# Optimization experiments

Hardware: AMD Instinct MI355X
Metric: run time of the kernel (lower is better)

Reference implementation:

```python
import jax, jax.numpy as jnp
import numpy as np

FEATURES_DIM = 64 * (64 * 10 + 1)  # 41024
BASE = 64 * 10 + 1                 # 641
B = 1024


def encode_boards(boards):
    """Vectorized HalfKP encode. boards: [B,8,8] int in 0..12.
    0 = my king, 12 = opp king, 6 = empty, 1..5 my pieces, 7..11 opp pieces.
    Returns [B, 2*FEATURES_DIM] float32 = concat(opps, mys) per original code."""
    nb = boards.shape[0]
    d = boards.reshape(nb, 64)
    sq = jnp.arange(64, dtype=jnp.int32)
    my_king = jnp.argmax(d == 0, axis=1).astype(jnp.int32)    # [B]
    opp_king = jnp.argmax(d == 12, axis=1).astype(jnp.int32)  # [B]
    is_my = (d >= 1) & (d <= 5)
    is_opp = (d >= 7) & (d <= 11)
    # MY_PIECE_TYPES index = piece-1 ; OPP_PIECE_TYPES [11,10,9,8,7] index = 11-piece
    my_idx = my_king[:, None] * BASE + (d - 1) * 64 + sq
    opp_idx = opp_king[:, None] * BASE + (11 - d) * 64 + sq
    my_idx = jnp.where(is_my, my_idx, FEATURES_DIM)    # out-of-range -> dropped
    opp_idx = jnp.where(is_opp, opp_idx, FEATURES_DIM)
    rows = jnp.arange(nb)[:, None]
    mys = jnp.zeros((nb, FEATURES_DIM), jnp.float32).at[rows, my_idx].set(1.0, mode='drop')
    opps = jnp.zeros((nb, FEATURES_DIM), jnp.float32).at[rows, opp_idx].set(1.0, mode='drop')
    return jnp.concatenate([opps, mys], axis=1)


def setup_inputs() -> dict:
    key = jax.random.key(0)
    ks = jax.random.split(key, 12)
    # boards: values 1..11 everywhere, then place exactly one my-king (0) and one opp-king (12)
    bf = jax.random.randint(ks[0], (B, 64), 1, 12, dtype=jnp.int32)
    mk = jax.random.randint(ks[1], (B,), 0, 32)
    ok = jax.random.randint(ks[2], (B,), 32, 64)
    rows = jnp.arange(B)
    bf = bf.at[rows, mk].set(0).at[rows, ok].set(12)
    boards = bf.reshape(B, 8, 8)
    s = 0.02
    W_my = jax.random.normal(ks[3], (256, FEATURES_DIM), jnp.float32) * s
    b_my = jax.random.normal(ks[4], (256,), jnp.float32) * s
    W_opp = jax.random.normal(ks[5], (256, FEATURES_DIM), jnp.float32) * s
    b_opp = jax.random.normal(ks[6], (256,), jnp.float32) * s
    W1 = jax.random.normal(ks[7], (32, 512), jnp.float32) * s
    b1 = jnp.zeros((32,), jnp.float32)
    W2 = jax.random.normal(ks[8], (32, 32), jnp.float32) * s
    b2 = jnp.zeros((32,), jnp.float32)
    W3 = jax.random.normal(ks[9], (1, 32), jnp.float32) * s
    b3 = jnp.zeros((1,), jnp.float32)
    return {"boards": boards, "W_my": W_my, "b_my": b_my, "W_opp": W_opp,
            "b_opp": b_opp, "W1": W1, "b1": b1, "W2": W2, "b2": b2,
            "W3": W3, "b3": b3}


def reference(boards, W_my, b_my, W_opp, b_opp, W1, b1, W2, b2, W3, b3):
    feats = encode_boards(boards)              # [B, 2*FEATURES_DIM] = (opps, mys)
    # NOTE: faithful to original: my_pieces consumes the FIRST half (which is opps)
    my_in = feats[:, :FEATURES_DIM]
    opp_in = feats[:, FEATURES_DIM:]
    my_pos = jax.nn.relu(my_in @ W_my.T + b_my)     # [B,256]
    opp_pos = jax.nn.relu(opp_in @ W_opp.T + b_opp) # [B,256]
    h = jnp.concatenate([my_pos, opp_pos], axis=1)  # [B,512]
    h = jax.nn.relu(h @ W1.T + b1)
    h = jax.nn.relu(h @ W2.T + b2)
    out = h @ W3.T + b3                             # [B,1]
    return out.reshape(-1)
```

## Files before the change

### kernel.cpp

```cpp
#include <hip/hip_runtime.h>

#define FD     41024
#define KBASE  641
#define WIN    320
#define SLDS   324
#define NB_MAX 1024

#define WS_OFF0  0
#define WS_OFF1  (NB_MAX*64)
#define WS_N0    (2*NB_MAX*64)
#define WS_N1    (WS_N0 + NB_MAX)
#define WS_KMY   (WS_N1 + NB_MAX)
#define WS_KOPP  (WS_KMY + NB_MAX)
#define WS_H     (WS_KOPP + NB_MAX)

__global__ __launch_bounds__(64) void classify(
    const int* __restrict__ boards, int* __restrict__ ws)
{
    __shared__ int s_off0[64], s_off1[64];
    __shared__ int s_cnt[2], s_k[2];
    const int b = blockIdx.x;
    const int t = threadIdx.x;

    s_off0[t] = 0; s_off1[t] = 0;
    if (t < 2) s_cnt[t] = 0;
    __syncthreads();

    const int d = boards[b * 64 + t];
    if (d == 0)       s_k[0] = t;
    else if (d == 12) s_k[1] = t;
    else if (d >= 1 && d <= 5) { int p = atomicAdd(&s_cnt[1], 1); s_off1[p] = (d - 1) * 64 + t; }
    else if (d >= 7 && d <= 11){ int p = atomicAdd(&s_cnt[0], 1); s_off0[p] = (11 - d) * 64 + t; }
    __syncthreads();

    ws[WS_OFF0 + b * 64 + t] = s_off0[t];
    ws[WS_OFF1 + b * 64 + t] = s_off1[t];
    if (t == 0) {
        ws[WS_N0   + b] = s_cnt[0];
        ws[WS_N1   + b] = s_cnt[1];
        ws[WS_KMY  + b] = s_k[0];
        ws[WS_KOPP + b] = s_k[1];
    }
}

__global__ __launch_bounds__(256) void gather_bucketed(
    const float* __restrict__ W_my, const float* __restrict__ W_opp,
    const float* __restrict__ b_my, const float* __restrict__ b_opp,
    const int* __restrict__ ws, float* __restrict__ h, int nb)
{
    __shared__ float win[32 * SLDS];
    __shared__ int   s_list[NB_MAX];
    __shared__ int   goffs[8 * 64];
    __shared__ int   s_cnt;

    const int blk = blockIdx.x;
    const int rg  = blk & 7;
    const int k   = (blk >> 3) & 63;
    const int m   = blk >> 9;
    const int t   = threadIdx.x;

    if (t == 0) s_cnt = 0;
    __syncthreads();

    const int* __restrict__ karr = ws + (m ? WS_KMY : WS_KOPP);
    for (int i = t; i < nb; i += 256)
        if (karr[i] == k) { int p = atomicAdd(&s_cnt, 1); s_list[p] = i; }
    __syncthreads();

    const int n_b = s_cnt;
    if (n_b == 0) return;

    const int shift = (k * KBASE) & 3;
    const int cs    = k * KBASE - shift;
    const float* __restrict__ W = m ? W_opp : W_my;
    const size_t gbase = (size_t)(rg * 32) * FD + (size_t)cs;
    #pragma unroll
    for (int u = 0; u < 11; u++) {
        const int idx = u * 256 + t;
        if (idx < 2592) {
            const int r  = idx / 81;
            const int c4 = idx - r * 81;
            const float4 v = *(const float4*)(W + gbase + (size_t)r * FD + c4 * 4);
            *(float4*)(&win[r * SLDS + c4 * 4]) = v;
        }
    }
    __syncthreads();

    const int* __restrict__ offarr = ws + (m ? WS_OFF1 : WS_OFF0);
    const int* __restrict__ narr   = ws + (m ? WS_N1   : WS_N0);
    const int r    = t & 31;
    const int slot = t >> 5;
    const float bias = (m ? b_opp : b_my)[rg * 32 + r];
    const int hcol = m * 256 + rg * 32 + r;
    const float* __restrict__ wrow = &win[r * SLDS + shift];

    for (int g = 0; g < n_b; g += 8) {
        {
            const int j  = t;
            if (j < 128) {
                const int bi = g + (j >> 4);
                if (bi < n_b) {
                    const int4 v = *(const int4*)(offarr + s_list[bi] * 64 + (j & 15) * 4);
                    *(int4*)(&goffs[j * 4]) = v;
                }
            }
        }
        __syncthreads();

        const int bi = g + slot;
        if (bi < n_b) {
            const int board = s_list[bi];
            const int nf = narr[board];
            const int* __restrict__ lo = &goffs[slot * 64];
            float acc0 = 0.0f, acc1 = 0.0f;
            int i = 0;
            for (; i + 4 <= nf; i += 4) {
                acc0 += wrow[lo[i]]     + wrow[lo[i + 1]];
                acc1 += wrow[lo[i + 2]] + wrow[lo[i + 3]];
            }
            for (; i < nf; i++) acc0 += wrow[lo[i]];
            h[(size_t)board * 512 + hcol] = fmaxf(acc0 + acc1 + bias, 0.0f);
        }
        __syncthreads();
    }
}

__global__ __launch_bounds__(256) void mlp_tail(
    const float* __restrict__ h,
    const float* __restrict__ W1, const float* __restrict__ b1,
    const float* __restrict__ W2, const float* __restrict__ b2,
    const float* __restrict__ W3, const float* __restrict__ b3,
    float* __restrict__ out)
{
    __shared__ float s_h[512];
    __shared__ float s_h1[32];
    const int b = blockIdx.x;
    const int t = threadIdx.x;

    s_h[t]       = h[(size_t)b * 512 + t];
    s_h[256 + t] = h[(size_t)b * 512 + 256 + t];
    __syncthreads();

    {
        const int o = t >> 3, l = t & 7;
        const float* __restrict__ w = W1 + o * 512;
        float p = 0.0f;
        for (int kk = l; kk < 512; kk += 8) p += s_h[kk] * w[kk];
        p += __shfl_down(p, 4, 8);
        p += __shfl_down(p, 2, 8);
        p += __shfl_down(p, 1, 8);
        if (l == 0) s_h1[o] = fmaxf(p + b1[o], 0.0f);
    }
    __syncthreads();

    if (t < 32) {
        const float* __restrict__ w = W2 + t * 32;
        float acc = b2[t];
        for (int kk = 0; kk < 32; kk++) acc += s_h1[kk] * w[kk];
        float h2 = fmaxf(acc, 0.0f);
        float p = h2 * W3[t];
        p += __shfl_down(p, 16, 32);
        p += __shfl_down(p,  8, 32);
        p += __shfl_down(p,  4, 32);
        p += __shfl_down(p,  2, 32);
        p += __shfl_down(p,  1, 32);
        if (t == 0) out[b] = p + b3[0];
    }
}

__global__ __launch_bounds__(256) void nnue_fwd(
    const int*   __restrict__ boards,
    const float* __restrict__ W_my,  const float* __restrict__ b_my,
    const float* __restrict__ W_opp, const float* __restrict__ b_opp,
    const float* __restrict__ W1,    const float* __restrict__ b1,
    const float* __restrict__ W2,    const float* __restrict__ b2,
    const float* __restrict__ W3,    const float* __restrict__ b3,
    float* __restrict__ out)
{
    __shared__ int   s_off0[64], s_off1[64];
    __shared__ int   s_cnt[2], s_kings[2];
    __shared__ float s_h[512];
    __shared__ float s_h1[32];

    const int b = blockIdx.x;
    const int t = threadIdx.x;

    if (t < 2) s_cnt[t] = 0;
    __syncthreads();

    if (t < 64) {
        int d = boards[b * 64 + t];
        if (d == 0)       s_kings[0] = t;
        else if (d == 12) s_kings[1] = t;
        else if (d >= 1 && d <= 5) { int p = atomicAdd(&s_cnt[1], 1); s_off1[p] = (d - 1) * 64 + t; }
        else if (d >= 7)           { int p = atomicAdd(&s_cnt[0], 1); s_off0[p] = (11 - d) * 64 + t; }
    }
    __syncthreads();

    const int n0 = s_cnt[0], n1 = s_cnt[1];
    const int base0 = s_kings[1] * KBASE;
    const int base1 = s_kings[0] * KBASE;

    {
        const float* __restrict__ w = W_my + (size_t)t * FD + base0;
        float acc = b_my[t];
        for (int i = 0; i < n0; i++) acc += w[s_off0[i]];
        s_h[t] = fmaxf(acc, 0.0f);
    }
    {
        const float* __restrict__ w = W_opp + (size_t)t * FD + base1;
        float acc = b_opp[t];
        for (int i = 0; i < n1; i++) acc += w[s_off1[i]];
        s_h[256 + t] = fmaxf(acc, 0.0f);
    }
    __syncthreads();

    {
        const int o = t >> 3, l = t & 7;
        const float* __restrict__ w = W1 + o * 512;
        float p = 0.0f;
        for (int kk = l; kk < 512; kk += 8) p += s_h[kk] * w[kk];
        p += __shfl_down(p, 4, 8);
        p += __shfl_down(p, 2, 8);
        p += __shfl_down(p, 1, 8);
        if (l == 0) s_h1[o] = fmaxf(p + b1[o], 0.0f);
    }
    __syncthreads();

    if (t < 32) {
        const float* __restrict__ w = W2 + t * 32;
        float acc = b2[t];
        for (int kk = 0; kk < 32; kk++) acc += s_h1[kk] * w[kk];
        float h2 = fmaxf(acc, 0.0f);
        float p = h2 * W3[t];
        p += __shfl_down(p, 16, 32);
        p += __shfl_down(p,  8, 32);
        p += __shfl_down(p,  4, 32);
        p += __shfl_down(p,  2, 32);
        p += __shfl_down(p,  1, 32);
        if (t == 0) out[b] = p + b3[0];
    }
}

extern "C" void kernel_launch(void* const* d_in, const int* in_sizes, int n_in,
                              void* d_out, int out_size, void* d_ws, size_t ws_size,
                              hipStream_t stream) {
    const int*   boards = (const int*)  d_in[0];
    const float* W_my   = (const float*)d_in[1];
    const float* b_my   = (const float*)d_in[2];
    const float* W_opp  = (const float*)d_in[3];
    const float* b_opp  = (const float*)d_in[4];
    const float* W1     = (const float*)d_in[5];
    const float* b1     = (const float*)d_in[6];
    const float* W2     = (const float*)d_in[7];
    const float* b2     = (const float*)d_in[8];
    const float* W3     = (const float*)d_in[9];
    const float* b3     = (const float*)d_in[10];
    float* out = (float*)d_out;

    const int nb = in_sizes[0] / 64;
    const size_t ws_needed = (size_t)(WS_H + (size_t)NB_MAX * 512) * sizeof(int);

    if (nb <= NB_MAX && ws_size >= ws_needed) {
        int*   wsi = (int*)d_ws;
        float* h   = (float*)d_ws + WS_H;
        classify<<<nb, 64, 0, stream>>>(boards, wsi);
        gather_bucketed<<<1024, 256, 0, stream>>>(W_my, W_opp, b_my, b_opp, wsi, h, nb);
        mlp_tail<<<nb, 256, 0, stream>>>(h, W1, b1, W2, b2, W3, b3, out);
    } else {
        nnue_fwd<<<nb, 256, 0, stream>>>(boards, W_my, b_my, W_opp, b_opp,
                                         W1, b1, W2, b2, W3, b3, out);
    }
}
```

Measured before the change: 145.5 us.

## Halve row group per block and prefetch weight window before bucket scan

Each gather block now covers 16 weight rows instead of 32, so twice as many blocks launch (2048) and each stages a smaller LDS window and processes 16 boards per group. The weight-window global loads are issued into registers before the king-bucket scan, so their latency overlaps the list build rather than following it. The cost is more blocks each re-scanning the king array and loading board offsets, extra registers for the prefetched float4s, and loads issued even for blocks that then exit with an empty bucket.

```diff
diff --git a/kernel.cpp b/kernel.cpp
--- a/kernel.cpp
+++ b/kernel.cpp
@@ -4,6 +4,7 @@
 #define KBASE  641
 #define WIN    320
 #define SLDS   324
+#define ROWG   16
 #define NB_MAX 1024
 
 #define WS_OFF0  0
@@ -48,20 +49,35 @@
     const float* __restrict__ b_my, const float* __restrict__ b_opp,
     const int* __restrict__ ws, float* __restrict__ h, int nb)
 {
-    __shared__ float win[32 * SLDS];
+    __shared__ float win[ROWG * SLDS];
     __shared__ int   s_list[NB_MAX];
-    __shared__ int   goffs[8 * 64];
+    __shared__ int   goffs[16 * 64];
     __shared__ int   s_cnt;
 
     const int blk = blockIdx.x;
-    const int rg  = blk & 7;
-    const int k   = (blk >> 3) & 63;
-    const int m   = blk >> 9;
+    const int rg  = blk & 15;
+    const int k   = (blk >> 4) & 63;
+    const int m   = blk >> 10;
     const int t   = threadIdx.x;
 
+    const int shift = (k * KBASE) & 3;
+    const int cs    = k * KBASE - shift;
+    const float* __restrict__ W = m ? W_opp : W_my;
+    const size_t gbase = (size_t)(rg * ROWG) * FD + (size_t)cs;
+    float4 v[6];
+    int    vidx[6];
+    #pragma unroll
+    for (int u = 0; u < 6; u++) {
+        int idx = u * 256 + t;
+        vidx[u] = idx;
+        if (idx > 1295) idx = 1295;
+        const int r  = idx / 81;
+        const int c4 = idx - r * 81;
+        v[u] = *(const float4*)(W + gbase + (size_t)r * FD + c4 * 4);
+    }
+
     if (t == 0) s_cnt = 0;
     __syncthreads();
-
     const int* __restrict__ karr = ws + (m ? WS_KMY : WS_KOPP);
     for (int i = t; i < nb; i += 256)
         if (karr[i] == k) { int p = atomicAdd(&s_cnt, 1); s_list[p] = i; }
@@ -70,39 +86,31 @@
     const int n_b = s_cnt;
     if (n_b == 0) return;
 
-    const int shift = (k * KBASE) & 3;
-    const int cs    = k * KBASE - shift;
-    const float* __restrict__ W = m ? W_opp : W_my;
-    const size_t gbase = (size_t)(rg * 32) * FD + (size_t)cs;
     #pragma unroll
-    for (int u = 0; u < 11; u++) {
-        const int idx = u * 256 + t;
-        if (idx < 2592) {
+    for (int u = 0; u < 6; u++) {
+        const int idx = vidx[u];
+        if (idx < 1296) {
             const int r  = idx / 81;
             const int c4 = idx - r * 81;
-            const float4 v = *(const float4*)(W + gbase + (size_t)r * FD + c4 * 4);
-            *(float4*)(&win[r * SLDS + c4 * 4]) = v;
+            *(float4*)(&win[r * SLDS + c4 * 4]) = v[u];
         }
     }
     __syncthreads();
 
     const int* __restrict__ offarr = ws + (m ? WS_OFF1 : WS_OFF0);
     const int* __restrict__ narr   = ws + (m ? WS_N1   : WS_N0);
-    const int r    = t & 31;
-    const int slot = t >> 5;
-    const float bias = (m ? b_opp : b_my)[rg * 32 + r];
-    const int hcol = m * 256 + rg * 32 + r;
+    const int r    = t & 15;
+    const int slot = t >> 4;
+    const float bias = (m ? b_opp : b_my)[rg * ROWG + r];
+    const int hcol = m * 256 + rg * ROWG + r;
     const float* __restrict__ wrow = &win[r * SLDS + shift];
 
-    for (int g = 0; g < n_b; g += 8) {
+    for (int g = 0; g < n_b; g += 16) {
         {
-            const int j  = t;
-            if (j < 128) {
-                const int bi = g + (j >> 4);
-                if (bi < n_b) {
-                    const int4 v = *(const int4*)(offarr + s_list[bi] * 64 + (j & 15) * 4);
-                    *(int4*)(&goffs[j * 4]) = v;
-                }
+            const int bi = g + (t >> 4);
+            if (bi < n_b) {
+                const int4 o4 = *(const int4*)(offarr + s_list[bi] * 64 + (t & 15) * 4);
+                *(int4*)(&goffs[(t >> 4) * 64 + (t & 15) * 4]) = o4;
             }
         }
         __syncthreads();
@@ -265,7 +273,7 @@
         int*   wsi = (int*)d_ws;
         float* h   = (float*)d_ws + WS_H;
         classify<<<nb, 64, 0, stream>>>(boards, wsi);
-        gather_bucketed<<<1024, 256, 0, stream>>>(W_my, W_opp, b_my, b_opp, wsi, h, nb);
+        gather_bucketed<<<2048, 256, 0, stream>>>(W_my, W_opp, b_my, b_opp, wsi, h, nb);
         mlp_tail<<<nb, 256, 0, stream>>>(h, W1, b1, W2, b2, W3, b3, out);
     } else {
         nnue_fwd<<<nb, 256, 0, stream>>>(boards, W_my, b_my, W_opp, b_opp,
```

Result: slower. 154.7 us (+6.3%).
